# Kernel tuning notes

Hardware: AMD Instinct MI355X
Metric: run time of the kernel (lower is better)

The kernel has to match this reference:

```python
import jax, jax.numpy as jnp
import numpy as np

EMBED_DIM = 1024
NUM_HEADS = 16
HEAD_DIM = EMBED_DIM // NUM_HEADS
SCALING = HEAD_DIM ** -0.5
EPS = 1e-5


def _rope(seq_len):
    inv_freq = 1.0 / (10000.0 ** (jnp.arange(0, HEAD_DIM, 2, dtype=jnp.float32) / HEAD_DIM))
    freqs = jnp.arange(seq_len, dtype=jnp.float32)[:, None] * inv_freq[None, :]
    emb = jnp.concatenate([freqs, freqs], axis=-1)  # (S, HEAD_DIM)
    return jnp.cos(emb), jnp.sin(emb)


def _rotate(x, cos, sin):
    # x: (B,H,S,Dh), cos/sin: (S,Dh)
    d = x.shape[-1]
    x1, x2 = x[..., : d // 2], x[..., d // 2 :]
    rotated = jnp.concatenate([-x2, x1], axis=-1)
    return x * cos + rotated * sin


def setup_inputs() -> dict:
    key = jax.random.key(0)
    ks = jax.random.split(key, 6)
    B, S, D = 2, 2048, EMBED_DIM
    scale = D ** -0.5
    return {
        "x": jax.random.normal(ks[0], (B, S, D), jnp.float32),
        "Wq": jax.random.normal(ks[1], (D, D), jnp.float32) * scale,
        "Wk": jax.random.normal(ks[2], (D, D), jnp.float32) * scale,
        "Wv": jax.random.normal(ks[3], (D, D), jnp.float32) * scale,
        "Wg": jax.random.normal(ks[4], (D, D), jnp.float32) * scale,
        "Wo": jax.random.normal(ks[5], (D, D), jnp.float32) * scale,
        "gn_w": jnp.ones((D,), jnp.float32),
        "gn_b": jnp.zeros((D,), jnp.float32),
    }


def reference(x, Wq, Wk, Wv, Wg, Wo, gn_w, gn_b):
    B, S, D = x.shape
    H, Dh = NUM_HEADS, HEAD_DIM

    def split_heads(t):  # (B,S,D) -> (B,H,S,Dh)
        return t.reshape(B, S, H, Dh).transpose(0, 2, 1, 3)

    q = split_heads(x @ Wq.T)
    k = split_heads(x @ Wk.T)
    v = split_heads(x @ Wv.T)

    cos, sin = _rope(S)
    q = _rotate(q, cos, sin)
    k = _rotate(k, cos, sin)

    retention = jnp.einsum("bhsd,bhtd->bhst", q, k) * SCALING

    # multiplicative causal decay mask: gamma**(n-m) for n>=m else 0
    gammas = (1.0 - 2.0 ** (-5.0 - jnp.arange(H, dtype=jnp.float32)))  # (H,)
    diff = jnp.arange(S)[:, None] - jnp.arange(S)[None, :]             # (S,S)
    causal = diff >= 0
    decay = jnp.where(causal, gammas[:, None, None] ** jnp.maximum(diff, 0).astype(jnp.float32), 0.0)  # (H,S,S)
    retention = retention * decay[None]

    out = jnp.einsum("bhst,bhtd->bhsd", retention, v)  # (B,H,S,Dh)
    out = out.transpose(0, 2, 1, 3).reshape(B * S, H, Dh)

    # GroupNorm with num_groups == H over channel dim D
    mean = out.mean(axis=-1, keepdims=True)
    var = out.var(axis=-1, keepdims=True)
    out = (out - mean) * jax.lax.rsqrt(var + EPS)
    out = out * gn_w.reshape(H, Dh) + gn_b.reshape(H, Dh)
    out = out.reshape(B, S, D)

    gate = jax.nn.silu(x @ Wg.T)
    return (gate * out) @ Wo.T
```

## Files before the change

kernel.cpp:

```cpp
#include <hip/hip_runtime.h>
#include <cstdint>
#include <cstddef>


typedef __attribute__((ext_vector_type(4))) float  f32x4;
typedef __attribute__((ext_vector_type(8))) short  bf16x8;
typedef __attribute__((ext_vector_type(4))) short  bf16x4v;
typedef __attribute__((ext_vector_type(2))) unsigned int u32x2;

#define MFMA_BF16 __builtin_amdgcn_mfma_f32_16x16x32_bf16

#define GLL16(gp, lp) __builtin_amdgcn_global_load_lds( \
    (const __attribute__((address_space(1))) unsigned int*)(const void*)(gp), \
    (__attribute__((address_space(3))) unsigned int*)(void*)(lp), 16, 0, 0)

__device__ __forceinline__ unsigned short f2bf(float f) {
    unsigned u = __float_as_uint(f);
    u += 0x7fffu + ((u >> 16) & 1u);
    return (unsigned short)(u >> 16);
}
__device__ __forceinline__ float bf2f(unsigned short h) {
    return __uint_as_float(((unsigned)h) << 16);
}
__device__ __forceinline__ unsigned cvt_pk_bf16(float lo, float hi) {
    unsigned r;
    asm("v_cvt_pk_bf16_f32 %0, %1, %2" : "=v"(r) : "v"(lo), "v"(hi));
    return r;
}

__global__ void convert_kernel(const float* __restrict__ x,
                               const float* __restrict__ wq, const float* __restrict__ wk,
                               const float* __restrict__ wv, const float* __restrict__ wg,
                               const float* __restrict__ wo,
                               unsigned short* __restrict__ dst,
                               float* __restrict__ cosT, float* __restrict__ sinT) {
    const size_t total = 4194304u + 5u * 1048576u;
    for (size_t i = (size_t)blockIdx.x * blockDim.x + threadIdx.x;
         i * 4 < total; i += (size_t)gridDim.x * blockDim.x) {
        size_t e = i * 4;
        const float* src; size_t off;
        if (e < 4194304u) { src = x; off = e; }
        else {
            size_t r = e - 4194304u;
            int w = (int)(r >> 20); off = r & 1048575u;
            src = (w == 0) ? wq : (w == 1) ? wk : (w == 2) ? wv : (w == 3) ? wg : wo;
        }
        f32x4 v = *(const f32x4*)(src + off);
        unsigned short o0 = f2bf(v[0]), o1 = f2bf(v[1]), o2 = f2bf(v[2]), o3 = f2bf(v[3]);
        unsigned long long pack = (unsigned long long)o0 | ((unsigned long long)o1 << 16)
                                | ((unsigned long long)o2 << 32) | ((unsigned long long)o3 << 48);
        *(unsigned long long*)(dst + e) = pack;
    }
    if (blockIdx.x < 256) {
        int i = blockIdx.x * 256 + threadIdx.x;
        int s = i >> 5, j = i & 31;
        float inv = exp2f(-(float)j * (13.287712379549449f / 32.0f));
        float ang = (float)s * inv;
        cosT[i] = cosf(ang);
        sinT[i] = sinf(ang);
    }
}

template<int NI>
__launch_bounds__(256, NI == 4 ? 2 : 3)
__global__ void gemm_fused(const unsigned short* __restrict__ A_x,
                           const unsigned short* __restrict__ A_a2,
                           const unsigned short* __restrict__ Wq, const unsigned short* __restrict__ Wk,
                           const unsigned short* __restrict__ Wv, const unsigned short* __restrict__ Wg,
                           const unsigned short* __restrict__ Wo,
                           const float* __restrict__ cosT, const float* __restrict__ sinT,
                           unsigned short* __restrict__ q_hm, unsigned short* __restrict__ k_hm,
                           unsigned short* __restrict__ kTs, unsigned short* __restrict__ vT,
                           unsigned short* __restrict__ gate,
                           float* __restrict__ outf,
                           int mode_base) {
    constexpr int BROWS = NI * 32;

    int flat = (blockIdx.z * gridDim.y + blockIdx.y) * gridDim.x + blockIdx.x;
    int nwg  = gridDim.z * gridDim.y * gridDim.x;
    int L    = (flat & 7) * (nwg >> 3) + (flat >> 3);

    int mode, m0, n0;
    if (NI == 4) {
        mode = mode_base + (L >> 8);
        int rem = L & 255;
        m0 = (rem >> 3) * 128;
        n0 = (rem & 7) * 128;
    } else {
        mode = mode_base;
        m0 = (L >> 4) * 128;
        n0 = (L & 15) * 64;
    }

    const unsigned short* A = (mode == 4) ? A_a2 : A_x;
    const unsigned short* W = (mode == 0) ? Wq : (mode == 1) ? Wk :
                              (mode == 2) ? Wv : (mode == 3) ? Wg : Wo;

    __shared__ __align__(16) unsigned short Ash[2][128 * 64];
    __shared__ __align__(16) unsigned short Bsh[2][BROWS * 64];

    int tid = threadIdx.x;
    int lane = tid & 63, wid = tid >> 6;
    int wm = wid >> 1, wn = wid & 1;

    int l_row = lane >> 3;
    int l_src = ((lane & 7) ^ l_row) << 3;
    const unsigned short* Ab = A + (size_t)(m0 + wid * 32 + l_row) * 1024 + l_src;
    const unsigned short* Wb = W + (size_t)(n0 + wid * (BROWS / 4) + l_row) * 1024 + l_src;

    f32x4 acc[4][NI];
#pragma unroll
    for (int i = 0; i < 4; ++i)
#pragma unroll
        for (int j = 0; j < NI; ++j)
#pragma unroll
            for (int r = 0; r < 4; ++r) acc[i][j][r] = 0.0f;

    auto stage = [&](int buf, int k0) {
#pragma unroll
        for (int i = 0; i < 4; ++i)
            GLL16(Ab + (size_t)(i * 8) * 1024 + k0, &Ash[buf][(wid * 32 + i * 8) * 64]);
#pragma unroll
        for (int i = 0; i < NI; ++i)
            GLL16(Wb + (size_t)(i * 8) * 1024 + k0, &Bsh[buf][(wid * (BROWS / 4) + i * 8) * 64]);
    };

    auto compute = [&](int buf) {
#pragma unroll
        for (int ks = 0; ks < 2; ++ks) {
            bf16x8 af[4], bfv[NI];
            int c = ks * 4 + (lane >> 4);
#pragma unroll
            for (int mi = 0; mi < 4; ++mi) {
                int row = wm * 64 + mi * 16 + (lane & 15);
                af[mi] = *(const bf16x8*)&Ash[buf][row * 64 + ((c ^ (row & 7)) << 3)];
            }
#pragma unroll
            for (int ni = 0; ni < NI; ++ni) {
                int row = wn * (BROWS / 2) + ni * 16 + (lane & 15);
                bfv[ni] = *(const bf16x8*)&Bsh[buf][row * 64 + ((c ^ (row & 7)) << 3)];
            }
            __builtin_amdgcn_s_setprio(1);
            if (mode == 2) {
#pragma unroll
                for (int mi = 0; mi < 4; ++mi)
#pragma unroll
                    for (int ni = 0; ni < NI; ++ni)
                        acc[mi][ni] = MFMA_BF16(bfv[ni], af[mi], acc[mi][ni], 0, 0, 0);
            } else {
#pragma unroll
                for (int mi = 0; mi < 4; ++mi)
#pragma unroll
                    for (int ni = 0; ni < NI; ++ni)
                        acc[mi][ni] = MFMA_BF16(af[mi], bfv[ni], acc[mi][ni], 0, 0, 0);
            }
            __builtin_amdgcn_s_setprio(0);
        }
    };

    stage(0, 0);
    asm volatile("s_waitcnt vmcnt(0)" ::: "memory");
    __syncthreads();

    for (int t = 0; t < 15; ++t) {
        int cur = t & 1;
        stage(cur ^ 1, (t + 1) * 64);
        compute(cur);
        asm volatile("s_waitcnt vmcnt(0)" ::: "memory");
        __syncthreads();
    }
    compute(1);

    int mbase = m0 + wm * 64, nbase = n0 + wn * (BROWS / 2);
    int g4 = (lane >> 4) << 2;

    if constexpr (NI == 4) {
        if (mode == 0 || mode == 1) {
            unsigned short* dst = (mode == 0) ? q_hm : k_hm;
            float sr[4] = {1.f, 1.f, 1.f, 1.f}, m16p[4] = {1.f, 1.f, 1.f, 1.f};
            if (mode == 1) {
                float lg = log2f(1.0f - exp2f(-5.0f - (float)(nbase >> 6)));
                float gm1 = exp2f(-lg), gm16 = exp2f(-16.0f * lg);
                sr[0] = exp2f(lg * (float)(63 - g4));
                sr[1] = sr[0] * gm1; sr[2] = sr[1] * gm1; sr[3] = sr[2] * gm1;
                m16p[1] = gm16; m16p[2] = gm16 * gm16; m16p[3] = m16p[2] * gm16;
            }
#pragma unroll
            for (int mi = 0; mi < 4; ++mi)
#pragma unroll
                for (int ni = 0; ni < 4; ++ni)
#pragma unroll
                    for (int r = 0; r < 4; ++r) {
                        int m = mbase + mi * 16 + g4 + r;
                        int n = nbase + ni * 16 + (lane & 15);
                        int s = m & 2047, b = m >> 11, h = n >> 6, d = n & 63, j = d & 31;
                        float v  = acc[mi][ni][r];
                        float v2 = acc[mi][ni ^ 2][r];
                        float cs = cosT[s * 32 + j], sn = sinT[s * 32 + j];
                        float rot = (d < 32) ? -v2 : v2;
                        float o = v * cs + rot * sn;
                        dst[((size_t)(b * 16 + h) * 2048 + s) * 64 + d] = f2bf(o);
                        if (mode == 1) {
                            kTs[((size_t)((b * 16 + h) * 64 + d)) * 2048 + s]
                                = f2bf(o * (sr[r] * m16p[mi]));
                        }
                    }
        } else if (mode == 2) {
#pragma unroll
            for (int mi = 0; mi < 4; ++mi)
#pragma unroll
                for (int ni = 0; ni < 4; ++ni)
#pragma unroll
                    for (int r = 0; r < 4; ++r) {
                        int n = nbase + ni * 16 + g4 + r;
                        int m = mbase + mi * 16 + (lane & 15);
                        int b = m >> 11, s = m & 2047, h = n >> 6, d = n & 63;
                        vT[((size_t)((b * 16 + h) * 64 + d)) * 2048 + s] = f2bf(acc[mi][ni][r]);
                    }
        } else {
#pragma unroll
            for (int mi = 0; mi < 4; ++mi)
#pragma unroll
                for (int ni = 0; ni < 4; ++ni)
#pragma unroll
                    for (int r = 0; r < 4; ++r) {
                        int m = mbase + mi * 16 + g4 + r;
                        int n = nbase + ni * 16 + (lane & 15);
                        float v = acc[mi][ni][r];
                        gate[(size_t)m * 1024 + n] = f2bf(v / (1.0f + expf(-v)));
                    }
        }
    } else {
#pragma unroll
        for (int mi = 0; mi < 4; ++mi)
#pragma unroll
            for (int ni = 0; ni < NI; ++ni)
#pragma unroll
                for (int r = 0; r < 4; ++r) {
                    int m = mbase + mi * 16 + g4 + r;
                    int n = nbase + ni * 16 + (lane & 15);
                    outf[(size_t)m * 1024 + n] = acc[mi][ni][r];
                }
    }
}

__launch_bounds__(256, 4)
__global__ void chunk_state_kernel(const unsigned short* __restrict__ vT,
                                   const unsigned short* __restrict__ kTs,
                                   unsigned short* __restrict__ LT) {
    int tid = threadIdx.x, lane = tid & 63, wid = tid >> 6;
    int bh = blockIdx.x >> 3;
    int c  = (blockIdx.x & 7) * 4 + wid;
    int q_lane = lane & 15;
    int g4 = (lane >> 4) << 2, g8 = (lane >> 4) << 3;

    const unsigned short* vb = vT  + (size_t)bh * 131072 + (size_t)c * 64;
    const unsigned short* kb = kTs + (size_t)bh * 131072 + (size_t)c * 64;

    f32x4 acc[4][4];
#pragma unroll
    for (int i = 0; i < 4; ++i)
#pragma unroll
        for (int j = 0; j < 4; ++j)
#pragma unroll
            for (int r = 0; r < 4; ++r) acc[i][j][r] = 0.0f;

#pragma unroll
    for (int ks = 0; ks < 2; ++ks) {
        bf16x8 a[4], bv[4];
#pragma unroll
        for (int mi = 0; mi < 4; ++mi)
            a[mi] = *(const bf16x8*)(vb + (size_t)(mi * 16 + q_lane) * 2048 + ks * 32 + g8);
#pragma unroll
        for (int ni = 0; ni < 4; ++ni)
            bv[ni] = *(const bf16x8*)(kb + (size_t)(ni * 16 + q_lane) * 2048 + ks * 32 + g8);
#pragma unroll
        for (int mi = 0; mi < 4; ++mi)
#pragma unroll
            for (int ni = 0; ni < 4; ++ni)
                acc[mi][ni] = MFMA_BF16(a[mi], bv[ni], acc[mi][ni], 0, 0, 0);
    }

    unsigned short* lp = LT + ((size_t)(bh * 32 + c)) * 4096;
#pragma unroll
    for (int mi = 0; mi < 4; ++mi)
#pragma unroll
        for (int ni = 0; ni < 4; ++ni)
#pragma unroll
            for (int r = 0; r < 4; ++r) {
                int d2 = mi * 16 + g4 + r;
                int d1 = ni * 16 + q_lane;
                lp[d2 * 64 + d1] = f2bf(acc[mi][ni][r]);
            }
}

__launch_bounds__(256, 4)
__global__ void scan_kernel(const unsigned short* __restrict__ LT,
                            unsigned short* __restrict__ ST) {
    int bh = blockIdx.x >> 2;
    int e0 = ((blockIdx.x & 3) * 256 + threadIdx.x) * 4;
    int h = bh & 15;
    float lg2g = log2f(1.0f - exp2f(-5.0f - (float)h));
    float g64 = exp2f(64.0f * lg2g);

    float s0 = 0.f, s1 = 0.f, s2 = 0.f, s3 = 0.f;
    const unsigned short* lp = LT + (size_t)bh * 32 * 4096 + e0;
    unsigned short* sp = ST + (size_t)bh * 32 * 4096 + e0;
    for (int c = 0; c < 32; ++c) {
        u32x2 wv;
        wv[0] = cvt_pk_bf16(s0, s1);
        wv[1] = cvt_pk_bf16(s2, s3);
        *(u32x2*)sp = wv;
        bf16x4v lv = *(const bf16x4v*)lp;
        s0 = s0 * g64 + bf2f((unsigned short)lv[0]);
        s1 = s1 * g64 + bf2f((unsigned short)lv[1]);
        s2 = s2 * g64 + bf2f((unsigned short)lv[2]);
        s3 = s3 * g64 + bf2f((unsigned short)lv[3]);
        lp += 4096; sp += 4096;
    }
}

__launch_bounds__(256, 4)
__global__ void retention_chunk_kernel(const unsigned short* __restrict__ qh,
                                       const unsigned short* __restrict__ kh,
                                       const unsigned short* __restrict__ vT,
                                       const unsigned short* __restrict__ ST,
                                       const float* __restrict__ gn_w, const float* __restrict__ gn_b,
                                       const unsigned short* __restrict__ gate,
                                       unsigned short* __restrict__ a2) {
    __shared__ __align__(16) unsigned short Ssh[4][16 * 40];

    int tid = threadIdx.x, lane = tid & 63, wid = tid >> 6;
    int c = blockIdx.x, bh = blockIdx.y;
    int b = bh >> 4, h = bh & 15;

    float lg2g = log2f(1.0f - exp2f(-5.0f - (float)h));
    float gam1 = exp2f(lg2g);
    float gmr1 = exp2f(-lg2g);
    float gmr2 = gmr1 * gmr1, gmr3 = gmr2 * gmr1;
    float gmr16 = exp2f(-16.0f * lg2g);

    int q_lane = lane & 15;
    int g4 = (lane >> 4) << 2, g8 = (lane >> 4) << 3;
    int i_col = wid * 16 + q_lane;
    int s_abs = c * 64 + i_col;

    bf16x8 aq0, aq1;
    {
        const unsigned short* qp = qh + ((size_t)bh * 2048 + s_abs) * 64 + g8;
        aq0 = *(const bf16x8*)(qp);
        aq1 = *(const bf16x8*)(qp + 32);
    }

    f32x4 z4 = {0.f, 0.f, 0.f, 0.f};
    f32x4 o0, o1, o2, o3;

    {
        const unsigned short* stp = ST + ((size_t)(bh * 32 + c)) * 4096
                                  + (size_t)q_lane * 64 + g8;
        bf16x8 s00 = *(const bf16x8*)(stp);
        bf16x8 s01 = *(const bf16x8*)(stp + 32);
        bf16x8 s10 = *(const bf16x8*)(stp + 1024);
        bf16x8 s11 = *(const bf16x8*)(stp + 1056);
        bf16x8 s20 = *(const bf16x8*)(stp + 2048);
        bf16x8 s21 = *(const bf16x8*)(stp + 2080);
        bf16x8 s30 = *(const bf16x8*)(stp + 3072);
        bf16x8 s31 = *(const bf16x8*)(stp + 3104);
        o0 = MFMA_BF16(aq0, s00, z4, 0, 0, 0); o0 = MFMA_BF16(aq1, s01, o0, 0, 0, 0);
        o1 = MFMA_BF16(aq0, s10, z4, 0, 0, 0); o1 = MFMA_BF16(aq1, s11, o1, 0, 0, 0);
        o2 = MFMA_BF16(aq0, s20, z4, 0, 0, 0); o2 = MFMA_BF16(aq1, s21, o2, 0, 0, 0);
        o3 = MFMA_BF16(aq0, s30, z4, 0, 0, 0); o3 = MFMA_BF16(aq1, s31, o3, 0, 0, 0);
    }
    {
        float cs0 = 0.125f * exp2f(lg2g * (float)(wid * 16 + g4 + 1));
        float cs1 = cs0 * gam1, cs2 = cs1 * gam1, cs3 = cs2 * gam1;
        o0[0] *= cs0; o0[1] *= cs1; o0[2] *= cs2; o0[3] *= cs3;
        o1[0] *= cs0; o1[1] *= cs1; o1[2] *= cs2; o1[3] *= cs3;
        o2[0] *= cs0; o2[1] *= cs1; o2[2] *= cs2; o2[3] *= cs3;
        o3[0] *= cs0; o3[1] *= cs1; o3[2] *= cs2; o3[3] *= cs3;
    }

    const unsigned short* kbase = kh + ((size_t)bh * 2048 + c * 64) * 64;
    const unsigned short* vbase = vT + (size_t)bh * 131072 + c * 64;
    unsigned short* ssw = &Ssh[wid][0];
    int ntt = (wid >> 1) + 1;
    for (int tt = 0; tt < ntt; ++tt) {
        int tbase = tt * 32;
        const unsigned short* kp = kbase + (size_t)(tbase + q_lane) * 64 + g8;
        bf16x8 k00 = *(const bf16x8*)(kp);
        bf16x8 k01 = *(const bf16x8*)(kp + 32);
        bf16x8 k10 = *(const bf16x8*)(kp + 1024);
        bf16x8 k11 = *(const bf16x8*)(kp + 1056);
        f32x4 sc0 = z4, sc1 = z4;
        sc0 = MFMA_BF16(k00, aq0, sc0, 0, 0, 0);
        sc0 = MFMA_BF16(k01, aq1, sc0, 0, 0, 0);
        sc1 = MFMA_BF16(k10, aq0, sc1, 0, 0, 0);
        sc1 = MFMA_BF16(k11, aq1, sc1, 0, 0, 0);

        int j0 = tbase + g4;
        float e0 = 0.125f * exp2f(lg2g * (float)(i_col - j0));
        float e1 = e0 * gmr1, e2 = e0 * gmr2, e3 = e0 * gmr3;
        float v00 = (i_col >= j0    ) ? sc0[0] * e0 : 0.0f;
        float v01 = (i_col >= j0 + 1) ? sc0[1] * e1 : 0.0f;
        float v02 = (i_col >= j0 + 2) ? sc0[2] * e2 : 0.0f;
        float v03 = (i_col >= j0 + 3) ? sc0[3] * e3 : 0.0f;
        int j1 = j0 + 16;
        float f0 = e0 * gmr16, f1 = e1 * gmr16, f2 = e2 * gmr16, f3 = e3 * gmr16;
        float v10 = (i_col >= j1    ) ? sc1[0] * f0 : 0.0f;
        float v11 = (i_col >= j1 + 1) ? sc1[1] * f1 : 0.0f;
        float v12 = (i_col >= j1 + 2) ? sc1[2] * f2 : 0.0f;
        float v13 = (i_col >= j1 + 3) ? sc1[3] * f3 : 0.0f;

        u32x2 wA, wB;
        wA[0] = cvt_pk_bf16(v00, v01); wA[1] = cvt_pk_bf16(v02, v03);
        wB[0] = cvt_pk_bf16(v10, v11); wB[1] = cvt_pk_bf16(v12, v13);
        *(u32x2*)&ssw[q_lane * 40 + g4] = wA;
        *(u32x2*)&ssw[q_lane * 40 + 16 + g4] = wB;

        bf16x8 sf = *(const bf16x8*)&ssw[q_lane * 40 + g8];
        bf16x8 bv0 = *(const bf16x8*)(vbase + (size_t)(q_lane) * 2048 + tbase + g8);
        bf16x8 bv1 = *(const bf16x8*)(vbase + (size_t)(16 + q_lane) * 2048 + tbase + g8);
        bf16x8 bv2 = *(const bf16x8*)(vbase + (size_t)(32 + q_lane) * 2048 + tbase + g8);
        bf16x8 bv3 = *(const bf16x8*)(vbase + (size_t)(48 + q_lane) * 2048 + tbase + g8);
        o0 = MFMA_BF16(sf, bv0, o0, 0, 0, 0);
        o1 = MFMA_BF16(sf, bv1, o1, 0, 0, 0);
        o2 = MFMA_BF16(sf, bv2, o2, 0, 0, 0);
        o3 = MFMA_BF16(sf, bv3, o3, 0, 0, 0);
    }

    float mean[4], rstd[4];
#pragma unroll
    for (int r = 0; r < 4; ++r) {
        float s1 = o0[r] + o1[r] + o2[r] + o3[r];
        float s2 = o0[r]*o0[r] + o1[r]*o1[r] + o2[r]*o2[r] + o3[r]*o3[r];
#pragma unroll
        for (int m = 1; m < 16; m <<= 1) {
            s1 += __shfl_xor(s1, m);
            s2 += __shfl_xor(s2, m);
        }
        float mu = s1 * 0.015625f;
        mean[r] = mu;
        float var = s2 * 0.015625f - mu * mu;
        rstd[r] = rsqrtf(var + 1e-5f);
    }
    int srow = c * 64 + wid * 16;
#define RT_STORE(OV, DB)                                                    \
    {                                                                       \
        int d = DB * 16 + q_lane;                                           \
        float gw = gn_w[h * 64 + d];                                        \
        float gb = gn_b[h * 64 + d];                                        \
        _Pragma("unroll")                                                   \
        for (int r = 0; r < 4; ++r) {                                       \
            int s_out = srow + g4 + r;                                      \
            size_t gi = ((size_t)(b * 2048 + s_out)) * 1024 + h * 64 + d;   \
            float val = (OV[r] - mean[r]) * rstd[r] * gw + gb;              \
            val *= bf2f(gate[gi]);                                          \
            a2[gi] = f2bf(val);                                             \
        }                                                                   \
    }
    RT_STORE(o0, 0); RT_STORE(o1, 1); RT_STORE(o2, 2); RT_STORE(o3, 3);
#undef RT_STORE
}

extern "C" void kernel_launch(void* const* d_in, const int* in_sizes, int n_in,
                              void* d_out, int out_size, void* d_ws, size_t ws_size,
                              hipStream_t stream) {
    const float* x    = (const float*)d_in[0];
    const float* Wq   = (const float*)d_in[1];
    const float* Wk   = (const float*)d_in[2];
    const float* Wv   = (const float*)d_in[3];
    const float* Wg   = (const float*)d_in[4];
    const float* Wo   = (const float*)d_in[5];
    const float* gn_w = (const float*)d_in[6];
    const float* gn_b = (const float*)d_in[7];

    unsigned short* xb   = (unsigned short*)d_ws;
    unsigned short* wqb  = xb  + 4194304;
    unsigned short* wkb  = wqb + 1048576;
    unsigned short* wvb  = wkb + 1048576;
    unsigned short* wgb  = wvb + 1048576;
    unsigned short* wob  = wgb + 1048576;
    float*          cosT = (float*)(wob + 1048576);
    float*          sinT = cosT + 65536;
    unsigned short* q_hm = (unsigned short*)(sinT + 65536);
    unsigned short* k_hm = q_hm + 4194304;
    unsigned short* vTb  = k_hm + 4194304;
    unsigned short* kTs  = vTb + 4194304;
    unsigned short* a2   = kTs + 4194304;
    unsigned short* gate = a2  + 4194304;
    unsigned short* LT   = a2;
    unsigned short* ST   = xb;

    float* outf = (float*)d_out;

    convert_kernel<<<dim3(2048), dim3(256), 0, stream>>>(
        x, Wq, Wk, Wv, Wg, Wo, xb, cosT, sinT);
    gemm_fused<4><<<dim3(8, 32, 4), dim3(256), 0, stream>>>(
        xb, a2, wqb, wkb, wvb, wgb, wob, cosT, sinT,
        q_hm, k_hm, kTs, vTb, gate, outf, 0);
    chunk_state_kernel<<<dim3(256), dim3(256), 0, stream>>>(vTb, kTs, LT);
    scan_kernel<<<dim3(128), dim3(256), 0, stream>>>(LT, ST);
    retention_chunk_kernel<<<dim3(32, 32), dim3(256), 0, stream>>>(
        q_hm, k_hm, vTb, ST, gn_w, gn_b, gate, a2);
    gemm_fused<2><<<dim3(16, 32, 1), dim3(256), 0, stream>>>(
        xb, a2, wqb, wkb, wvb, wgb, wob, cosT, sinT,
        q_hm, k_hm, kTs, vTb, gate, outf, 4);
}
```

Measured before the change: 132.3 us.

## Use 256x256-tile, 8-wave projection GEMM with deeper async prefetch pipeline

Replaces the templated 128x128 projection GEMM with a dedicated 512-thread kernel that computes 256x256 output tiles. It prefetches two K-stages ahead with partial vmcnt waits and inserts barriers inside compute. The larger tile raises arithmetic intensity and cuts redundant global loads of A and W. The output GEMM becomes a separate, specialised kernel. In exchange the grid has only 256 blocks, the register and LDS footprint grows (64KB+ LDS, 128 accumulator regs), and there is extra barrier overhead.

```diff
diff --git a/kernel.cpp b/kernel.cpp
--- a/kernel.cpp
+++ b/kernel.cpp
@@ -13,6 +13,9 @@
 #define GLL16(gp, lp) __builtin_amdgcn_global_load_lds( \
     (const __attribute__((address_space(1))) unsigned int*)(const void*)(gp), \
     (__attribute__((address_space(3))) unsigned int*)(void*)(lp), 16, 0, 0)
+
+#define WAITV(N) asm volatile("s_waitcnt vmcnt(" #N ")" ::: "memory")
+#define BARRIER  asm volatile("s_barrier" ::: "memory")
 
 __device__ __forceinline__ unsigned short f2bf(float f) {
     unsigned u = __float_as_uint(f);
@@ -61,58 +64,192 @@
     }
 }
 
-template<int NI>
-__launch_bounds__(256, NI == 4 ? 2 : 3)
-__global__ void gemm_fused(const unsigned short* __restrict__ A_x,
-                           const unsigned short* __restrict__ A_a2,
-                           const unsigned short* __restrict__ Wq, const unsigned short* __restrict__ Wk,
-                           const unsigned short* __restrict__ Wv, const unsigned short* __restrict__ Wg,
-                           const unsigned short* __restrict__ Wo,
-                           const float* __restrict__ cosT, const float* __restrict__ sinT,
-                           unsigned short* __restrict__ q_hm, unsigned short* __restrict__ k_hm,
-                           unsigned short* __restrict__ kTs, unsigned short* __restrict__ vT,
-                           unsigned short* __restrict__ gate,
-                           float* __restrict__ outf,
-                           int mode_base) {
-    constexpr int BROWS = NI * 32;
-
-    int flat = (blockIdx.z * gridDim.y + blockIdx.y) * gridDim.x + blockIdx.x;
-    int nwg  = gridDim.z * gridDim.y * gridDim.x;
-    int L    = (flat & 7) * (nwg >> 3) + (flat >> 3);
-
-    int mode, m0, n0;
-    if (NI == 4) {
-        mode = mode_base + (L >> 8);
-        int rem = L & 255;
-        m0 = (rem >> 3) * 128;
-        n0 = (rem & 7) * 128;
+__launch_bounds__(512, 2)
+__global__ void gemm256_proj(const unsigned short* __restrict__ A_x,
+                             const unsigned short* __restrict__ Wq, const unsigned short* __restrict__ Wk,
+                             const unsigned short* __restrict__ Wv, const unsigned short* __restrict__ Wg,
+                             const float* __restrict__ cosT, const float* __restrict__ sinT,
+                             unsigned short* __restrict__ q_hm, unsigned short* __restrict__ k_hm,
+                             unsigned short* __restrict__ kTs, unsigned short* __restrict__ vT,
+                             unsigned short* __restrict__ gate) {
+    int mode = blockIdx.z;
+    const unsigned short* W = (mode == 0) ? Wq : (mode == 1) ? Wk :
+                              (mode == 2) ? Wv : Wg;
+
+    __shared__ __align__(16) unsigned short Ash[2][256 * 64];
+    __shared__ __align__(16) unsigned short Bsh[2][256 * 64];
+
+    int tid = threadIdx.x;
+    int lane = tid & 63, wid = tid >> 6;
+    int wr = wid >> 2, wc = wid & 3;
+    int m0 = blockIdx.y * 256, n0 = blockIdx.x * 256;
+    int q_lane = lane & 15;
+
+    int s_row = tid >> 3;
+    int s_c   = ((tid & 7) ^ (s_row & 7)) << 3;
+    const unsigned short* Ab = A_x + (size_t)(m0 + s_row) * 1024 + s_c;
+    const unsigned short* Wb = W   + (size_t)(n0 + s_row) * 1024 + s_c;
+
+    f32x4 acc[8][4];
+#pragma unroll
+    for (int i = 0; i < 8; ++i)
+#pragma unroll
+        for (int j = 0; j < 4; ++j)
+#pragma unroll
+            for (int r = 0; r < 4; ++r) acc[i][j][r] = 0.0f;
+
+    auto stage = [&](int p, int t) {
+        int k0 = t * 64;
+#pragma unroll
+        for (int i = 0; i < 4; ++i)
+            GLL16(Ab + (size_t)(i * 64) * 1024 + k0, &Ash[p][(i * 64 + wid * 8) * 64]);
+#pragma unroll
+        for (int i = 0; i < 4; ++i)
+            GLL16(Wb + (size_t)(i * 64) * 1024 + k0, &Bsh[p][(i * 64 + wid * 8) * 64]);
+    };
+
+    auto compute = [&](int p) {
+#pragma unroll
+        for (int q = 0; q < 4; ++q) {
+            const int mi0 = (q >> 1) * 4, ni0 = (q & 1) * 2;
+            bf16x8 af[4][2], bfv[2][2];
+#pragma unroll
+            for (int mi = 0; mi < 4; ++mi)
+#pragma unroll
+                for (int ks = 0; ks < 2; ++ks) {
+                    int row = wr * 128 + (mi0 + mi) * 16 + q_lane;
+                    int c = ks * 4 + (lane >> 4);
+                    af[mi][ks] = *(const bf16x8*)&Ash[p][row * 64 + ((c ^ (row & 7)) << 3)];
+                }
+#pragma unroll
+            for (int ni = 0; ni < 2; ++ni)
+#pragma unroll
+                for (int ks = 0; ks < 2; ++ks) {
+                    int row = wc * 64 + (ni0 + ni) * 16 + q_lane;
+                    int c = ks * 4 + (lane >> 4);
+                    bfv[ni][ks] = *(const bf16x8*)&Bsh[p][row * 64 + ((c ^ (row & 7)) << 3)];
+                }
+            BARRIER;
+            __builtin_amdgcn_s_setprio(1);
+            if (mode == 2) {
+#pragma unroll
+                for (int mi = 0; mi < 4; ++mi)
+#pragma unroll
+                    for (int ni = 0; ni < 2; ++ni)
+#pragma unroll
+                        for (int ks = 0; ks < 2; ++ks)
+                            acc[mi0 + mi][ni0 + ni] =
+                                MFMA_BF16(bfv[ni][ks], af[mi][ks], acc[mi0 + mi][ni0 + ni], 0, 0, 0);
+            } else {
+#pragma unroll
+                for (int mi = 0; mi < 4; ++mi)
+#pragma unroll
+                    for (int ni = 0; ni < 2; ++ni)
+#pragma unroll
+                        for (int ks = 0; ks < 2; ++ks)
+                            acc[mi0 + mi][ni0 + ni] =
+                                MFMA_BF16(af[mi][ks], bfv[ni][ks], acc[mi0 + mi][ni0 + ni], 0, 0, 0);
+            }
+            __builtin_amdgcn_s_setprio(0);
+            BARRIER;
+        }
+    };
+
+    stage(0, 0);
+    stage(1, 1);
+
+    for (int t = 0; t < 15; ++t) {
+        WAITV(8);
+        BARRIER;
+        compute(t & 1);
+        if (t < 14) stage(t & 1, t + 2);
+    }
+    WAITV(0);
+    BARRIER;
+    compute(1);
+
+    int mbase = m0 + wr * 128, nbase = n0 + wc * 64;
+    int g4 = (lane >> 4) << 2;
+
+    if (mode == 0 || mode == 1) {
+        unsigned short* dst = (mode == 0) ? q_hm : k_hm;
+        float sr[4] = {1.f, 1.f, 1.f, 1.f}, m16p[4] = {1.f, 1.f, 1.f, 1.f};
+        if (mode == 1) {
+            float lg = log2f(1.0f - exp2f(-5.0f - (float)(nbase >> 6)));
+            float gm1 = exp2f(-lg), gm16 = exp2f(-16.0f * lg);
+            sr[0] = exp2f(lg * (float)(63 - g4));
+            sr[1] = sr[0] * gm1; sr[2] = sr[1] * gm1; sr[3] = sr[2] * gm1;
+            m16p[1] = gm16; m16p[2] = gm16 * gm16; m16p[3] = m16p[2] * gm16;
+        }
+#pragma unroll
+        for (int mi = 0; mi < 8; ++mi)
+#pragma unroll
+            for (int ni = 0; ni < 4; ++ni)
+#pragma unroll
+                for (int r = 0; r < 4; ++r) {
+                    int m = mbase + mi * 16 + g4 + r;
+                    int n = nbase + ni * 16 + q_lane;
+                    int s = m & 2047, b = m >> 11, h = n >> 6, d = n & 63, j = d & 31;
+                    float v  = acc[mi][ni][r];
+                    float v2 = acc[mi][ni ^ 2][r];
+                    float cs = cosT[s * 32 + j], sn = sinT[s * 32 + j];
+                    float rot = (d < 32) ? -v2 : v2;
+                    float o = v * cs + rot * sn;
+                    dst[((size_t)(b * 16 + h) * 2048 + s) * 64 + d] = f2bf(o);
+                    if (mode == 1) {
+                        kTs[((size_t)((b * 16 + h) * 64 + d)) * 2048 + s]
+                            = f2bf(o * (sr[r] * m16p[mi & 3]));
+                    }
+                }
+    } else if (mode == 2) {
+#pragma unroll
+        for (int mi = 0; mi < 8; ++mi)
+#pragma unroll
+            for (int ni = 0; ni < 4; ++ni)
+#pragma unroll
+                for (int r = 0; r < 4; ++r) {
+                    int n = nbase + ni * 16 + g4 + r;
+                    int m = mbase + mi * 16 + q_lane;
+                    int b = m >> 11, s = m & 2047, h = n >> 6, d = n & 63;
+                    vT[((size_t)((b * 16 + h) * 64 + d)) * 2048 + s] = f2bf(acc[mi][ni][r]);
+                }
     } else {
-        mode = mode_base;
-        m0 = (L >> 4) * 128;
-        n0 = (L & 15) * 64;
-    }
-
-    const unsigned short* A = (mode == 4) ? A_a2 : A_x;
-    const unsigned short* W = (mode == 0) ? Wq : (mode == 1) ? Wk :
-                              (mode == 2) ? Wv : (mode == 3) ? Wg : Wo;
-
+#pragma unroll
+        for (int mi = 0; mi < 8; ++mi)
+#pragma unroll
+            for (int ni = 0; ni < 4; ++ni)
+#pragma unroll
+                for (int r = 0; r < 4; ++r) {
+                    int m = mbase + mi * 16 + g4 + r;
+                    int n = nbase + ni * 16 + q_lane;
+                    float v = acc[mi][ni][r];
+                    gate[(size_t)m * 1024 + n] = f2bf(v / (1.0f + expf(-v)));
+                }
+    }
+}
+
+__launch_bounds__(256, 3)
+__global__ void gemm_out(const unsigned short* __restrict__ A_a2,
+                         const unsigned short* __restrict__ Wo,
+                         float* __restrict__ outf) {
     __shared__ __align__(16) unsigned short Ash[2][128 * 64];
-    __shared__ __align__(16) unsigned short Bsh[2][BROWS * 64];
+    __shared__ __align__(16) unsigned short Bsh[2][64 * 64];
 
     int tid = threadIdx.x;
     int lane = tid & 63, wid = tid >> 6;
     int wm = wid >> 1, wn = wid & 1;
+    int m0 = blockIdx.y * 128, n0 = blockIdx.x * 64;
 
     int l_row = lane >> 3;
     int l_src = ((lane & 7) ^ l_row) << 3;
-    const unsigned short* Ab = A + (size_t)(m0 + wid * 32 + l_row) * 1024 + l_src;
-    const unsigned short* Wb = W + (size_t)(n0 + wid * (BROWS / 4) + l_row) * 1024 + l_src;
-
-    f32x4 acc[4][NI];
+    const unsigned short* Ab = A_a2 + (size_t)(m0 + wid * 32 + l_row) * 1024 + l_src;
+    const unsigned short* Wb = Wo   + (size_t)(n0 + wid * 16 + l_row) * 1024 + l_src;
+
+    f32x4 acc[4][2];
 #pragma unroll
     for (int i = 0; i < 4; ++i)
 #pragma unroll
-        for (int j = 0; j < NI; ++j)
+        for (int j = 0; j < 2; ++j)
 #pragma unroll
             for (int r = 0; r < 4; ++r) acc[i][j][r] = 0.0f;
 
@@ -121,14 +258,14 @@
         for (int i = 0; i < 4; ++i)
             GLL16(Ab + (size_t)(i * 8) * 1024 + k0, &Ash[buf][(wid * 32 + i * 8) * 64]);
 #pragma unroll
-        for (int i = 0; i < NI; ++i)
-            GLL16(Wb + (size_t)(i * 8) * 1024 + k0, &Bsh[buf][(wid * (BROWS / 4) + i * 8) * 64]);
+        for (int i = 0; i < 2; ++i)
+            GLL16(Wb + (size_t)(i * 8) * 1024 + k0, &Bsh[buf][(wid * 16 + i * 8) * 64]);
     };
 
     auto compute = [&](int buf) {
 #pragma unroll
         for (int ks = 0; ks < 2; ++ks) {
-            bf16x8 af[4], bfv[NI];
+            bf16x8 af[4], bfv[2];
             int c = ks * 4 + (lane >> 4);
 #pragma unroll
             for (int mi = 0; mi < 4; ++mi) {
@@ -136,112 +273,44 @@
                 af[mi] = *(const bf16x8*)&Ash[buf][row * 64 + ((c ^ (row & 7)) << 3)];
             }
 #pragma unroll
-            for (int ni = 0; ni < NI; ++ni) {
-                int row = wn * (BROWS / 2) + ni * 16 + (lane & 15);
+            for (int ni = 0; ni < 2; ++ni) {
+                int row = wn * 32 + ni * 16 + (lane & 15);
                 bfv[ni] = *(const bf16x8*)&Bsh[buf][row * 64 + ((c ^ (row & 7)) << 3)];
             }
             __builtin_amdgcn_s_setprio(1);
-            if (mode == 2) {
-#pragma unroll
-                for (int mi = 0; mi < 4; ++mi)
-#pragma unroll
-                    for (int ni = 0; ni < NI; ++ni)
-                        acc[mi][ni] = MFMA_BF16(bfv[ni], af[mi], acc[mi][ni], 0, 0, 0);
-            } else {
-#pragma unroll
-                for (int mi = 0; mi < 4; ++mi)
-#pragma unroll
-                    for (int ni = 0; ni < NI; ++ni)
-                        acc[mi][ni] = MFMA_BF16(af[mi], bfv[ni], acc[mi][ni], 0, 0, 0);
-            }
+#pragma unroll
+            for (int mi = 0; mi < 4; ++mi)
+#pragma unroll
+                for (int ni = 0; ni < 2; ++ni)
+                    acc[mi][ni] = MFMA_BF16(af[mi], bfv[ni], acc[mi][ni], 0, 0, 0);
             __builtin_amdgcn_s_setprio(0);
         }
     };
 
     stage(0, 0);
-    asm volatile("s_waitcnt vmcnt(0)" ::: "memory");
+    WAITV(0);
     __syncthreads();
-
     for (int t = 0; t < 15; ++t) {
         int cur = t & 1;
         stage(cur ^ 1, (t + 1) * 64);
         compute(cur);
-        asm volatile("s_waitcnt vmcnt(0)" ::: "memory");
+        WAITV(0);
         __syncthreads();
     }
     compute(1);
 
-    int mbase = m0 + wm * 64, nbase = n0 + wn * (BROWS / 2);
+    int mbase = m0 + wm * 64, nbase = n0 + wn * 32;
     int g4 = (lane >> 4) << 2;
-
-    if constexpr (NI == 4) {
-        if (mode == 0 || mode == 1) {
-            unsigned short* dst = (mode == 0) ? q_hm : k_hm;
-            float sr[4] = {1.f, 1.f, 1.f, 1.f}, m16p[4] = {1.f, 1.f, 1.f, 1.f};
-            if (mode == 1) {
-                float lg = log2f(1.0f - exp2f(-5.0f - (float)(nbase >> 6)));
-                float gm1 = exp2f(-lg), gm16 = exp2f(-16.0f * lg);
-                sr[0] = exp2f(lg * (float)(63 - g4));
-                sr[1] = sr[0] * gm1; sr[2] = sr[1] * gm1; sr[3] = sr[2] * gm1;
-                m16p[1] = gm16; m16p[2] = gm16 * gm16; m16p[3] = m16p[2] * gm16;
+#pragma unroll
+    for (int mi = 0; mi < 4; ++mi)
+#pragma unroll
+        for (int ni = 0; ni < 2; ++ni)
+#pragma unroll
+            for (int r = 0; r < 4; ++r) {
+                int m = mbase + mi * 16 + g4 + r;
+                int n = nbase + ni * 16 + (lane & 15);
+                outf[(size_t)m * 1024 + n] = acc[mi][ni][r];
             }
-#pragma unroll
-            for (int mi = 0; mi < 4; ++mi)
-#pragma unroll
-                for (int ni = 0; ni < 4; ++ni)
-#pragma unroll
-                    for (int r = 0; r < 4; ++r) {
-                        int m = mbase + mi * 16 + g4 + r;
-                        int n = nbase + ni * 16 + (lane & 15);
-                        int s = m & 2047, b = m >> 11, h = n >> 6, d = n & 63, j = d & 31;
-                        float v  = acc[mi][ni][r];
-                        float v2 = acc[mi][ni ^ 2][r];
-                        float cs = cosT[s * 32 + j], sn = sinT[s * 32 + j];
-                        float rot = (d < 32) ? -v2 : v2;
-                        float o = v * cs + rot * sn;
-                        dst[((size_t)(b * 16 + h) * 2048 + s) * 64 + d] = f2bf(o);
-                        if (mode == 1) {
-                            kTs[((size_t)((b * 16 + h) * 64 + d)) * 2048 + s]
-                                = f2bf(o * (sr[r] * m16p[mi]));
-                        }
-                    }
-        } else if (mode == 2) {
-#pragma unroll
-            for (int mi = 0; mi < 4; ++mi)
-#pragma unroll
-                for (int ni = 0; ni < 4; ++ni)
-#pragma unroll
-                    for (int r = 0; r < 4; ++r) {
-                        int n = nbase + ni * 16 + g4 + r;
-                        int m = mbase + mi * 16 + (lane & 15);
-                        int b = m >> 11, s = m & 2047, h = n >> 6, d = n & 63;
-                        vT[((size_t)((b * 16 + h) * 64 + d)) * 2048 + s] = f2bf(acc[mi][ni][r]);
-                    }
-        } else {
-#pragma unroll
-            for (int mi = 0; mi < 4; ++mi)
-#pragma unroll
-                for (int ni = 0; ni < 4; ++ni)
-#pragma unroll
-                    for (int r = 0; r < 4; ++r) {
-                        int m = mbase + mi * 16 + g4 + r;
-                        int n = nbase + ni * 16 + (lane & 15);
-                        float v = acc[mi][ni][r];
-                        gate[(size_t)m * 1024 + n] = f2bf(v / (1.0f + expf(-v)));
-                    }
-        }
-    } else {
-#pragma unroll
-        for (int mi = 0; mi < 4; ++mi)
-#pragma unroll
-            for (int ni = 0; ni < NI; ++ni)
-#pragma unroll
-                for (int r = 0; r < 4; ++r) {
-                    int m = mbase + mi * 16 + g4 + r;
-                    int n = nbase + ni * 16 + (lane & 15);
-                    outf[(size_t)m * 1024 + n] = acc[mi][ni][r];
-                }
-    }
 }
 
 __launch_bounds__(256, 4)
@@ -495,14 +564,12 @@
 
     convert_kernel<<<dim3(2048), dim3(256), 0, stream>>>(
         x, Wq, Wk, Wv, Wg, Wo, xb, cosT, sinT);
-    gemm_fused<4><<<dim3(8, 32, 4), dim3(256), 0, stream>>>(
-        xb, a2, wqb, wkb, wvb, wgb, wob, cosT, sinT,
-        q_hm, k_hm, kTs, vTb, gate, outf, 0);
+    gemm256_proj<<<dim3(4, 16, 4), dim3(512), 0, stream>>>(
+        xb, wqb, wkb, wvb, wgb, cosT, sinT,
+        q_hm, k_hm, kTs, vTb, gate);
     chunk_state_kernel<<<dim3(256), dim3(256), 0, stream>>>(vTb, kTs, LT);
     scan_kernel<<<dim3(128), dim3(256), 0, stream>>>(LT, ST);
     retention_chunk_kernel<<<dim3(32, 32), dim3(256), 0, stream>>>(
         q_hm, k_hm, vTb, ST, gn_w, gn_b, gate, a2);
-    gemm_fused<2><<<dim3(16, 32, 1), dim3(256), 0, stream>>>(
-        xb, a2, wqb, wkb, wvb, wgb, wob, cosT, sinT,
-        q_hm, k_hm, kTs, vTb, gate, outf, 4);
-}
+    gemm_out<<<dim3(16, 32, 1), dim3(256), 0, stream>>>(a2, wob, outf);
+}
```

Result: slower. 136.5 us (+3.2%).
